# Kernel optimization log

Measured on AMD Instinct MI355X. Metric: run time of the kernel, lower is better.

Reference implementation:

```python
import jax, jax.numpy as jnp
import numpy as np

IN, OUT, RANK = 4096, 4096, 256
B_SZ, SEQ = 4, 2048


def setup_inputs() -> dict:
    key = jax.random.key(0)
    ks = jax.random.split(key, 6)
    x = jax.random.normal(ks[0], (B_SZ, SEQ, IN), dtype=jnp.float32)
    base_weight = jax.random.normal(ks[1], (OUT, IN), dtype=jnp.float32) * (1.0 / np.sqrt(IN))
    A = jax.random.normal(ks[2], (RANK, IN), dtype=jnp.float32) * (1.0 / np.sqrt(IN))
    B = jax.random.normal(ks[3], (OUT, RANK), dtype=jnp.float32) * (1.0 / np.sqrt(RANK))
    d = jax.random.normal(ks[4], (RANK,), dtype=jnp.float32)
    b = jax.random.normal(ks[5], (OUT,), dtype=jnp.float32)
    return {"x": x, "base_weight": base_weight, "A": A, "B": B, "d": d, "b": b}


def reference(x, base_weight, A, B, d, b):
    # base = F.linear(x, base_weight) = x @ base_weight^T
    base = jnp.einsum('bsi,oi->bso', x, base_weight)
    # Low-rank chain: x @ (B @ (d*A))^T == ((x @ A^T) * d) @ B^T  (same math,
    # avoids materializing the full out x in vera_weight)
    xa = jnp.einsum('bsi,ri->bsr', x, A) * d  # [B,S,rank]
    adaptation = jnp.einsum('bsr,or->bso', xa, B) + b
    return base + adaptation
```

## Files before the change

### kernel.cpp

```cpp
#include <hip/hip_runtime.h>
#include <hip/hip_bf16.h>
#include <cstdint>

typedef __bf16 bf16x8 __attribute__((ext_vector_type(8)));
typedef float  f32x4  __attribute__((ext_vector_type(4)));

typedef __attribute__((address_space(3))) void lds_void;
typedef const __attribute__((address_space(1))) void gbl_cvoid;

#define GLOAD_LDS16(g, l) \
    __builtin_amdgcn_global_load_lds((gbl_cvoid*)(g), (lds_void*)(l), 16, 0, 0)

static constexpr int IN   = 4096;
static constexpr int OUT  = 4096;
static constexpr int RANK = 256;
static constexpr int M_ROWS = 4 * 2048;

__device__ __forceinline__ void cast8(const float* __restrict__ in,
                                      __bf16* __restrict__ out, int t) {
    const float4* p = (const float4*)in + (size_t)t * 2;
    float4 v0 = p[0], v1 = p[1];
    bf16x8 o;
    o[0] = (__bf16)v0.x; o[1] = (__bf16)v0.y; o[2] = (__bf16)v0.z; o[3] = (__bf16)v0.w;
    o[4] = (__bf16)v1.x; o[5] = (__bf16)v1.y; o[6] = (__bf16)v1.z; o[7] = (__bf16)v1.w;
    ((bf16x8*)out)[t] = o;
}

__global__ __launch_bounds__(256) void prep(
    const float* __restrict__ Bm, __bf16* __restrict__ Bbf,
    const float* __restrict__ A,  const float* __restrict__ d,
    __bf16* __restrict__ AdT)
{
    __shared__ float tile[64][65];
    const int blk = blockIdx.x;
    const int t   = threadIdx.x;

    if (blk < 512) {
        cast8(Bm, Bbf, blk * 256 + t);
        return;
    }
    const int ab = blk - 512;
    const int i0 = (ab & 63) * 64;
    const int r0 = (ab >> 6) * 64;
    const int cl = t & 63;
    const int rw = t >> 6;

#pragma unroll
    for (int it = 0; it < 16; ++it) {
        int rl = it * 4 + rw;
        tile[rl][cl] = A[(size_t)(r0 + rl) * IN + i0 + cl];
    }
    __syncthreads();
    float dv = d[r0 + cl];
#pragma unroll
    for (int it = 0; it < 16; ++it) {
        int il = it * 4 + rw;
        AdT[(size_t)(i0 + il) * RANK + r0 + cl] = (__bf16)(tile[cl][il] * dv);
    }
}

__global__ __launch_bounds__(256) void castx(
    const float* __restrict__ x, __bf16* __restrict__ x_bf)
{
    for (int i = blockIdx.x * 256 + threadIdx.x; i < 4194304; i += 2048 * 256)
        cast8(x, x_bf, i);
}

__global__ __launch_bounds__(256) void weff(
    const __bf16* __restrict__ Bw,
    const __bf16* __restrict__ AdT,
    const float*  __restrict__ W,
    __bf16* __restrict__ Weff)
{
    __shared__ __bf16 sA[128 * 64];
    __shared__ __bf16 sB[128 * 64];

    const int blk = blockIdx.x;
    const int t   = threadIdx.x;

    constexpr int K = RANK;
    const int wave = t >> 6;
    const int lane = t & 63;
    const int quad = lane >> 4;
    const int l16  = lane & 15;
    const int m0 = (blk >> 5) * 128;
    const int n0 = (blk & 31) * 128;
    const int wm = (wave >> 1) * 64;
    const int wn = (wave & 1) * 64;
    const int xr = l16 & 7;

    f32x4 acc[4][4] = {};

    for (int kt = 0; kt < K; kt += 64) {
#pragma unroll
        for (int j = 0; j < 4; ++j) {
            int ci  = j * 256 + t;
            int row = ci >> 3;
            int kc  = (ci & 7) ^ (row & 7);
            GLOAD_LDS16(Bw  + (size_t)(m0 + row) * K + kt + kc * 8, sA + ci * 8);
        }
#pragma unroll
        for (int j = 0; j < 4; ++j) {
            int ci  = j * 256 + t;
            int row = ci >> 3;
            int kc  = (ci & 7) ^ (row & 7);
            GLOAD_LDS16(AdT + (size_t)(n0 + row) * K + kt + kc * 8, sB + ci * 8);
        }
        __syncthreads();

#pragma unroll
        for (int kk = 0; kk < 64; kk += 32) {
            const int kb = kk >> 3;
            bf16x8 a[4], b[4];
#pragma unroll
            for (int mi = 0; mi < 4; ++mi)
                a[mi] = *(const bf16x8*)(sA + (wm + mi * 16 + l16) * 64 + (((kb + quad) ^ xr) << 3));
#pragma unroll
            for (int ni = 0; ni < 4; ++ni)
                b[ni] = *(const bf16x8*)(sB + (wn + ni * 16 + l16) * 64 + (((kb + quad) ^ xr) << 3));
#pragma unroll
            for (int mi = 0; mi < 4; ++mi)
#pragma unroll
                for (int ni = 0; ni < 4; ++ni)
                    acc[mi][ni] = __builtin_amdgcn_mfma_f32_16x16x32_bf16(a[mi], b[ni], acc[mi][ni], 0, 0, 0);
        }
        __syncthreads();
    }

#pragma unroll
    for (int mi = 0; mi < 4; ++mi) {
#pragma unroll
        for (int r = 0; r < 4; ++r) {
            int row = m0 + wm + mi * 16 + quad * 4 + r;
#pragma unroll
            for (int ni = 0; ni < 4; ++ni) {
                int col = n0 + wn + ni * 16 + l16;
                size_t idx = (size_t)row * IN + col;
                Weff[idx] = (__bf16)(acc[mi][ni][r] + W[idx]);
            }
        }
    }
}


#define LD_A(BUF, mi) (*(const bf16x8*)&sX[BUF][abase + (mi) * 512])
#define LD_B(BUF, ni) (*(const bf16x8*)&sW[BUF][bbase + (ni) * 512])
#define BARR() __builtin_amdgcn_s_barrier()
#define VM(N)  asm volatile("s_waitcnt vmcnt(" #N ")")

#define STG_X(BUF, P) do { \
    GLOAD_LDS16((P),          &sX[BUF][tid * 8]); \
    GLOAD_LDS16((P) + 524288, &sX[BUF][4096 + tid * 8]); \
} while (0)
#define STG_W(BUF, P) do { \
    GLOAD_LDS16((P),          &sW[BUF][tid * 8]); \
    GLOAD_LDS16((P) + 524288, &sW[BUF][4096 + tid * 8]); \
} while (0)

#define MROW(mi, A, c0, c1, c2, c3) \
    acc[mi][0] = __builtin_amdgcn_mfma_f32_16x16x32_bf16(A, c0, acc[mi][0], 0, 0, 0); \
    acc[mi][1] = __builtin_amdgcn_mfma_f32_16x16x32_bf16(A, c1, acc[mi][1], 0, 0, 0); \
    acc[mi][2] = __builtin_amdgcn_mfma_f32_16x16x32_bf16(A, c2, acc[mi][2], 0, 0, 0); \
    acc[mi][3] = __builtin_amdgcn_mfma_f32_16x16x32_bf16(A, c3, acc[mi][3], 0, 0, 0);

#define TILE_NB(BUF) \
    { \
        bf16x8 a0 = LD_A(BUF, 0), a1 = LD_A(BUF, 1), a2 = LD_A(BUF, 2), a3 = LD_A(BUF, 3); \
        bf16x8 c0 = LD_B(BUF, 0), c1 = LD_B(BUF, 1), c2 = LD_B(BUF, 2), c3 = LD_B(BUF, 3); \
        __builtin_amdgcn_s_setprio(1); \
        MROW(0, a0, c0, c1, c2, c3) MROW(1, a1, c0, c1, c2, c3) \
        MROW(2, a2, c0, c1, c2, c3) MROW(3, a3, c0, c1, c2, c3) \
        __builtin_amdgcn_s_setprio(0); \
        a0 = LD_A(BUF, 4); a1 = LD_A(BUF, 5); a2 = LD_A(BUF, 6); a3 = LD_A(BUF, 7); \
        __builtin_amdgcn_s_setprio(1); \
        MROW(4, a0, c0, c1, c2, c3) MROW(5, a1, c0, c1, c2, c3) \
        MROW(6, a2, c0, c1, c2, c3) MROW(7, a3, c0, c1, c2, c3) \
        __builtin_amdgcn_s_setprio(0); \
    }

#define GRP(B0, B1, STGS) \
    { \
        VM(0); \
        BARR(); \
        __builtin_amdgcn_sched_barrier(0); \
        STGS; \
        TILE_NB(B0) \
        TILE_NB(B1) \
    }

__global__ __launch_bounds__(512, 2) void main_gemm(
    const __bf16* __restrict__ X,
    const __bf16* __restrict__ Wf,
    const float*  __restrict__ bias,
    float* __restrict__ out)
{
    constexpr int K = IN;
    constexpr int N = OUT;
    __shared__ __bf16 sX[4][8192];
    __shared__ __bf16 sW[4][8192];

    const int tid  = threadIdx.x;
    const int lane = tid & 63;
    const int quad = lane >> 4;
    const int l16  = lane & 15;
    const int wave = tid >> 6;
    const int wmb  = (wave >> 2) * 128;
    const int wnb  = (wave & 3) * 64;

    const int blk    = blockIdx.x;
    const int c      = blk & 7;
    const int i      = blk >> 3;
    const int n0     = (c * 2 + (i & 1)) * 256;
    const int m_base = (i >> 1) * 256;

    const int slot  = quad ^ ((l16 >> 1) & 3);
    const int abase = (wmb + l16) * 32 + slot * 8;
    const int bbase = (wnb + l16) * 32 + slot * 8;

    const int row0 = tid >> 2;
    const int ch0  = (tid & 3) ^ ((row0 >> 1) & 3);
    const __bf16* wsrc = Wf + (size_t)(n0 + row0) * K + ch0 * 8;

    float bv[4];
#pragma unroll
    for (int ni = 0; ni < 4; ++ni)
        bv[ni] = bias[n0 + wnb + ni * 16 + l16];

#pragma unroll 1
    for (int tp = 0; tp < 2; ++tp) {
        const int m0 = m_base + tp * 4096;
        const __bf16* xsrc = X + (size_t)(m0 + row0) * K + ch0 * 8;

        f32x4 acc[8][4] = {};

        STG_X(0, xsrc);      STG_W(0, wsrc);
        STG_X(1, xsrc + 32); STG_W(1, wsrc + 32);

        const __bf16* xs = xsrc + 64;
        const __bf16* ws = wsrc + 64;

#pragma unroll 1
        for (int it = 0; it < 31; ++it) {
            GRP(0, 1, STG_X(2, xs); STG_W(2, ws); STG_X(3, xs + 32); STG_W(3, ws + 32))
            GRP(2, 3, STG_X(0, xs + 64); STG_W(0, ws + 64); STG_X(1, xs + 96); STG_W(1, ws + 96))
            xs += 128; ws += 128;
        }

        GRP(0, 1, STG_X(2, xs); STG_W(2, ws); STG_X(3, xs + 32); STG_W(3, ws + 32))
        GRP(2, 3, (void)0)

#pragma unroll
        for (int mi = 0; mi < 8; ++mi) {
#pragma unroll
            for (int r = 0; r < 4; ++r) {
                int row = m0 + wmb + mi * 16 + quad * 4 + r;
#pragma unroll
                for (int ni = 0; ni < 4; ++ni) {
                    int col = n0 + wnb + ni * 16 + l16;
                    out[(size_t)row * N + col] = acc[mi][ni][r] + bv[ni];
                }
            }
        }
    }
}

#undef GRP
#undef TILE_NB
#undef MROW
#undef STG_X
#undef STG_W
#undef LD_A
#undef LD_B
#undef BARR
#undef VM

extern "C" void kernel_launch(void* const* d_in, const int* in_sizes, int n_in,
                              void* d_out, int out_size, void* d_ws, size_t ws_size,
                              hipStream_t stream) {
    const float* x  = (const float*)d_in[0];
    const float* W  = (const float*)d_in[1];
    const float* A  = (const float*)d_in[2];
    const float* Bm = (const float*)d_in[3];
    const float* d  = (const float*)d_in[4];
    const float* b  = (const float*)d_in[5];
    float* out = (float*)d_out;

    char* ws = (char*)d_ws;
    __bf16* x_bf   = (__bf16*)(ws);
    __bf16* weff_p = (__bf16*)(ws + (size_t)67108864);
    __bf16* b_bf   = (__bf16*)(ws + (size_t)67108864 + 33554432);
    __bf16* adt_bf = (__bf16*)(ws + (size_t)67108864 + 33554432 + 2097152);

    prep<<<768, 256, 0, stream>>>(Bm, b_bf, A, d, adt_bf);
    weff<<<1024, 256, 0, stream>>>(b_bf, adt_bf, W, weff_p);
    castx<<<2048, 256, 0, stream>>>(x, x_bf);
    main_gemm<<<256, 512, 0, stream>>>(x_bf, weff_p, b, out);
}
```

Measured before the change: 586.6 us.

## Switch main GEMM to 32x32x16 MFMA with 4 waves and register double-buffered fragments

Rewrites the main GEMM inner loop to use 32x32x16 bf16 MFMA instead of 16x16x32, and halves the block to 256 threads with 128x128 per-wave tiles. LDS fragments are prefetched into a ping-pong register set (p/q) so that reads for the next K-step overlap the current MFMAs. The global-to-LDS staging keeps 3 stages in flight using partial vmcnt waits instead of a full drain. The aim is fewer LDS reads per FLOP and better latency hiding, in exchange for much higher register pressure and lower wave occupancy.

```diff
diff --git a/kernel.cpp b/kernel.cpp
--- a/kernel.cpp
+++ b/kernel.cpp
@@ -4,6 +4,7 @@
 
 typedef __bf16 bf16x8 __attribute__((ext_vector_type(8)));
 typedef float  f32x4  __attribute__((ext_vector_type(4)));
+typedef float  f32x16 __attribute__((ext_vector_type(16)));
 
 typedef __attribute__((address_space(3))) void lds_void;
 typedef const __attribute__((address_space(1))) void gbl_cvoid;
@@ -143,52 +144,56 @@
 }
 
 
-#define LD_A(BUF, mi) (*(const bf16x8*)&sX[BUF][abase + (mi) * 512])
-#define LD_B(BUF, ni) (*(const bf16x8*)&sW[BUF][bbase + (ni) * 512])
+#define LDA(BUF, mi, SO) (*(const bf16x8*)&sX[BUF][arow + (mi) * 1024 + (SO)])
+#define LDB(BUF, ni, SO) (*(const bf16x8*)&sW[BUF][brow + (ni) * 1024 + (SO)])
 #define BARR() __builtin_amdgcn_s_barrier()
 #define VM(N)  asm volatile("s_waitcnt vmcnt(" #N ")")
 
 #define STG_X(BUF, P) do { \
-    GLOAD_LDS16((P),          &sX[BUF][tid * 8]); \
-    GLOAD_LDS16((P) + 524288, &sX[BUF][4096 + tid * 8]); \
+    GLOAD_LDS16((P),                  &sX[BUF][tid * 8]); \
+    GLOAD_LDS16((P) + (size_t)262144, &sX[BUF][2048 + tid * 8]); \
+    GLOAD_LDS16((P) + (size_t)524288, &sX[BUF][4096 + tid * 8]); \
+    GLOAD_LDS16((P) + (size_t)786432, &sX[BUF][6144 + tid * 8]); \
 } while (0)
 #define STG_W(BUF, P) do { \
-    GLOAD_LDS16((P),          &sW[BUF][tid * 8]); \
-    GLOAD_LDS16((P) + 524288, &sW[BUF][4096 + tid * 8]); \
+    GLOAD_LDS16((P),                  &sW[BUF][tid * 8]); \
+    GLOAD_LDS16((P) + (size_t)262144, &sW[BUF][2048 + tid * 8]); \
+    GLOAD_LDS16((P) + (size_t)524288, &sW[BUF][4096 + tid * 8]); \
+    GLOAD_LDS16((P) + (size_t)786432, &sW[BUF][6144 + tid * 8]); \
 } while (0)
 
-#define MROW(mi, A, c0, c1, c2, c3) \
-    acc[mi][0] = __builtin_amdgcn_mfma_f32_16x16x32_bf16(A, c0, acc[mi][0], 0, 0, 0); \
-    acc[mi][1] = __builtin_amdgcn_mfma_f32_16x16x32_bf16(A, c1, acc[mi][1], 0, 0, 0); \
-    acc[mi][2] = __builtin_amdgcn_mfma_f32_16x16x32_bf16(A, c2, acc[mi][2], 0, 0, 0); \
-    acc[mi][3] = __builtin_amdgcn_mfma_f32_16x16x32_bf16(A, c3, acc[mi][3], 0, 0, 0);
-
-#define TILE_NB(BUF) \
+#define MF(A, B, mi, ni) \
+    acc[mi][ni] = __builtin_amdgcn_mfma_f32_32x32x16_bf16(A, B, acc[mi][ni], 0, 0, 0);
+
+#define MHALF(A0, A1, A2, A3, B0, B1, B2, B3) \
+    MF(A0, B0, 0, 0) MF(A0, B1, 0, 1) MF(A0, B2, 0, 2) MF(A0, B3, 0, 3) \
+    MF(A1, B0, 1, 0) MF(A1, B1, 1, 1) MF(A1, B2, 1, 2) MF(A1, B3, 1, 3) \
+    MF(A2, B0, 2, 0) MF(A2, B1, 2, 1) MF(A2, B2, 2, 2) MF(A2, B3, 2, 3) \
+    MF(A3, B0, 3, 0) MF(A3, B1, 3, 1) MF(A3, B2, 3, 2) MF(A3, B3, 3, 3)
+
+#define RD8(RBUF, SO, A0, A1, A2, A3, B0, B1, B2, B3) \
+    A0 = LDA(RBUF, 0, SO); A1 = LDA(RBUF, 1, SO); \
+    A2 = LDA(RBUF, 2, SO); A3 = LDA(RBUF, 3, SO); \
+    B0 = LDB(RBUF, 0, SO); B1 = LDB(RBUF, 1, SO); \
+    B2 = LDB(RBUF, 2, SO); B3 = LDB(RBUF, 3, SO);
+
+#define TILE(RBUF, STGS, VMS, C, Nn) \
     { \
-        bf16x8 a0 = LD_A(BUF, 0), a1 = LD_A(BUF, 1), a2 = LD_A(BUF, 2), a3 = LD_A(BUF, 3); \
-        bf16x8 c0 = LD_B(BUF, 0), c1 = LD_B(BUF, 1), c2 = LD_B(BUF, 2), c3 = LD_B(BUF, 3); \
-        __builtin_amdgcn_s_setprio(1); \
-        MROW(0, a0, c0, c1, c2, c3) MROW(1, a1, c0, c1, c2, c3) \
-        MROW(2, a2, c0, c1, c2, c3) MROW(3, a3, c0, c1, c2, c3) \
-        __builtin_amdgcn_s_setprio(0); \
-        a0 = LD_A(BUF, 4); a1 = LD_A(BUF, 5); a2 = LD_A(BUF, 6); a3 = LD_A(BUF, 7); \
-        __builtin_amdgcn_s_setprio(1); \
-        MROW(4, a0, c0, c1, c2, c3) MROW(5, a1, c0, c1, c2, c3) \
-        MROW(6, a2, c0, c1, c2, c3) MROW(7, a3, c0, c1, c2, c3) \
-        __builtin_amdgcn_s_setprio(0); \
-    }
-
-#define GRP(B0, B1, STGS) \
-    { \
-        VM(0); \
+        VMS; \
         BARR(); \
         __builtin_amdgcn_sched_barrier(0); \
+        RD8(RBUF, s0, Nn##a0, Nn##a1, Nn##a2, Nn##a3, Nn##b0, Nn##b1, Nn##b2, Nn##b3) \
         STGS; \
-        TILE_NB(B0) \
-        TILE_NB(B1) \
-    }
-
-__global__ __launch_bounds__(512, 2) void main_gemm(
+        __builtin_amdgcn_s_setprio(1); \
+        MHALF(C##a0, C##a1, C##a2, C##a3, C##b0, C##b1, C##b2, C##b3) \
+        __builtin_amdgcn_s_setprio(0); \
+        RD8(RBUF, s1, Nn##a4, Nn##a5, Nn##a6, Nn##a7, Nn##b4, Nn##b5, Nn##b6, Nn##b7) \
+        __builtin_amdgcn_s_setprio(1); \
+        MHALF(C##a4, C##a5, C##a6, C##a7, C##b4, C##b5, C##b6, C##b7) \
+        __builtin_amdgcn_s_setprio(0); \
+    }
+
+__global__ __launch_bounds__(256, 1) void main_gemm(
     const __bf16* __restrict__ X,
     const __bf16* __restrict__ Wf,
     const float*  __restrict__ bias,
@@ -201,11 +206,11 @@
 
     const int tid  = threadIdx.x;
     const int lane = tid & 63;
-    const int quad = lane >> 4;
-    const int l16  = lane & 15;
+    const int r31  = lane & 31;
+    const int h    = lane >> 5;
     const int wave = tid >> 6;
-    const int wmb  = (wave >> 2) * 128;
-    const int wnb  = (wave & 3) * 64;
+    const int wmb  = (wave >> 1) * 128;
+    const int wnb  = (wave & 1) * 128;
 
     const int blk    = blockIdx.x;
     const int c      = blk & 7;
@@ -213,9 +218,11 @@
     const int n0     = (c * 2 + (i & 1)) * 256;
     const int m_base = (i >> 1) * 256;
 
-    const int slot  = quad ^ ((l16 >> 1) & 3);
-    const int abase = (wmb + l16) * 32 + slot * 8;
-    const int bbase = (wnb + l16) * 32 + slot * 8;
+    const int sz   = (r31 >> 1) & 3;
+    const int s0   = ((h ^ sz)) * 8;
+    const int s1   = (((2 + h) ^ sz)) * 8;
+    const int arow = (wmb + r31) * 32;
+    const int brow = (wnb + r31) * 32;
 
     const int row0 = tid >> 2;
     const int ch0  = (tid & 3) ^ ((row0 >> 1) & 3);
@@ -224,53 +231,72 @@
     float bv[4];
 #pragma unroll
     for (int ni = 0; ni < 4; ++ni)
-        bv[ni] = bias[n0 + wnb + ni * 16 + l16];
+        bv[ni] = bias[n0 + wnb + ni * 32 + r31];
 
 #pragma unroll 1
     for (int tp = 0; tp < 2; ++tp) {
         const int m0 = m_base + tp * 4096;
         const __bf16* xsrc = X + (size_t)(m0 + row0) * K + ch0 * 8;
 
-        f32x4 acc[8][4] = {};
+        f32x16 acc[4][4] = {};
+        bf16x8 pa0, pa1, pa2, pa3, pa4, pa5, pa6, pa7;
+        bf16x8 pb0, pb1, pb2, pb3, pb4, pb5, pb6, pb7;
+        bf16x8 qa0, qa1, qa2, qa3, qa4, qa5, qa6, qa7;
+        bf16x8 qb0, qb1, qb2, qb3, qb4, qb5, qb6, qb7;
 
         STG_X(0, xsrc);      STG_W(0, wsrc);
         STG_X(1, xsrc + 32); STG_W(1, wsrc + 32);
-
-        const __bf16* xs = xsrc + 64;
-        const __bf16* ws = wsrc + 64;
+        STG_X(2, xsrc + 64); STG_W(2, wsrc + 64);
+        VM(16);
+        BARR();
+        RD8(0, s0, pa0, pa1, pa2, pa3, pb0, pb1, pb2, pb3)
+        RD8(0, s1, pa4, pa5, pa6, pa7, pb4, pb5, pb6, pb7)
+
+        const __bf16* xs = xsrc + 96;
+        const __bf16* ws = wsrc + 96;
 
 #pragma unroll 1
         for (int it = 0; it < 31; ++it) {
-            GRP(0, 1, STG_X(2, xs); STG_W(2, ws); STG_X(3, xs + 32); STG_W(3, ws + 32))
-            GRP(2, 3, STG_X(0, xs + 64); STG_W(0, ws + 64); STG_X(1, xs + 96); STG_W(1, ws + 96))
+            TILE(1, STG_X(3, xs);      STG_W(3, ws),      VM(8), p, q)
+            TILE(2, STG_X(0, xs + 32); STG_W(0, ws + 32), VM(8), q, p)
+            TILE(3, STG_X(1, xs + 64); STG_W(1, ws + 64), VM(8), p, q)
+            TILE(0, STG_X(2, xs + 96); STG_W(2, ws + 96), VM(8), q, p)
             xs += 128; ws += 128;
         }
 
-        GRP(0, 1, STG_X(2, xs); STG_W(2, ws); STG_X(3, xs + 32); STG_W(3, ws + 32))
-        GRP(2, 3, (void)0)
-
-#pragma unroll
-        for (int mi = 0; mi < 8; ++mi) {
-#pragma unroll
-            for (int r = 0; r < 4; ++r) {
-                int row = m0 + wmb + mi * 16 + quad * 4 + r;
-#pragma unroll
-                for (int ni = 0; ni < 4; ++ni) {
-                    int col = n0 + wnb + ni * 16 + l16;
-                    out[(size_t)row * N + col] = acc[mi][ni][r] + bv[ni];
+        TILE(1, STG_X(3, xs); STG_W(3, ws), VM(8), p, q)
+        TILE(2, (void)0,                    VM(8), q, p)
+        TILE(3, (void)0,                    VM(0), p, q)
+        __builtin_amdgcn_s_setprio(1);
+        MHALF(qa0, qa1, qa2, qa3, qb0, qb1, qb2, qb3)
+        __builtin_amdgcn_s_setprio(0);
+        __builtin_amdgcn_s_setprio(1);
+        MHALF(qa4, qa5, qa6, qa7, qb4, qb5, qb6, qb7)
+        __builtin_amdgcn_s_setprio(0);
+
+#pragma unroll
+        for (int mi = 0; mi < 4; ++mi) {
+#pragma unroll
+            for (int ni = 0; ni < 4; ++ni) {
+#pragma unroll
+                for (int reg = 0; reg < 16; ++reg) {
+                    int row = m0 + wmb + mi * 32 + (reg & 3) + 8 * (reg >> 2) + 4 * h;
+                    int col = n0 + wnb + ni * 32 + r31;
+                    out[(size_t)row * N + col] = acc[mi][ni][reg] + bv[ni];
                 }
             }
         }
     }
 }
 
-#undef GRP
-#undef TILE_NB
-#undef MROW
+#undef TILE
+#undef RD8
+#undef MHALF
+#undef MF
 #undef STG_X
 #undef STG_W
-#undef LD_A
-#undef LD_B
+#undef LDA
+#undef LDB
 #undef BARR
 #undef VM
 
@@ -294,5 +320,5 @@
     prep<<<768, 256, 0, stream>>>(Bm, b_bf, A, d, adt_bf);
     weff<<<1024, 256, 0, stream>>>(b_bf, adt_bf, W, weff_p);
     castx<<<2048, 256, 0, stream>>>(x, x_bf);
-    main_gemm<<<256, 512, 0, stream>>>(x_bf, weff_p, b, out);
-}
+    main_gemm<<<256, 256, 0, stream>>>(x_bf, weff_p, b, out);
+}
```

Result: no change. 595.0 us (+1.4%).
